# Performance work log

Measured on AMD Instinct MI355X. Metric: run time of the kernel, lower is better.

The kernel has to match this reference:

```python
import math
import jax, jax.numpy as jnp
import numpy as np

FACTOR = 5


def setup_inputs() -> dict:
    key = jax.random.key(0)
    kq, kk, kv, ki = jax.random.split(key, 4)
    B, H, L, D = 4, 8, 2048, 64
    sample_k = min(FACTOR * math.ceil(math.log(L)), L)  # 40
    queries = jax.random.normal(kq, (B, H, L, D), dtype=jnp.float32)
    keys = jax.random.normal(kk, (B, H, L, D), dtype=jnp.float32)
    values = jax.random.normal(kv, (B, H, L, D), dtype=jnp.float32)
    index_sample = jax.random.randint(ki, (L, sample_k), 0, L, dtype=jnp.int64 if jax.config.jax_enable_x64 else jnp.int32)
    return {"queries": queries, "keys": keys, "values": values, "index_sample": index_sample}


def reference(queries, keys, values, index_sample):
    B, H, L_Q, D = queries.shape
    L_K = keys.shape[2]
    u = min(FACTOR * math.ceil(math.log(L_Q)), L_Q)  # n_top queries (= 40)
    scale = 1.0 / math.sqrt(D)

    # --- _prob_QK: sparsity measurement over randomly sampled keys ---
    # K_sample[b,h,q,s,:] = keys[b,h,index_sample[q,s],:]  -> [B,H,L_Q,S,D]
    K_sample = keys[:, :, index_sample, :]
    Q_K_sample = jnp.einsum('bhqd,bhqsd->bhqs', queries, K_sample)  # [B,H,L_Q,S]
    M = Q_K_sample.max(axis=-1) - Q_K_sample.sum(axis=-1) / L_K      # [B,H,L_Q]
    _, M_top = jax.lax.top_k(M, u)                                    # [B,H,u]

    Q_reduce = jnp.take_along_axis(queries, M_top[..., None], axis=2)  # [B,H,u,D]
    scores_top = jnp.einsum('bhud,bhkd->bhuk', Q_reduce, keys) * scale  # [B,H,u,L_K]

    # --- initial context: causal cumulative sum of V (mask_flag=True) ---
    context = jnp.cumsum(values, axis=2)  # [B,H,L_Q,D]

    # --- ProbMask: causal rows gathered at the selected query indices ---
    causal = jnp.triu(jnp.ones((L_Q, L_K), dtype=bool), 1)  # [L_Q,L_K]
    mask = causal[M_top]                                     # [B,H,u,L_K]
    scores_top = jnp.where(mask, -jnp.inf, scores_top)

    attn = jax.nn.softmax(scores_top, axis=-1)                       # [B,H,u,L_K]
    update = jnp.einsum('bhuk,bhkd->bhud', attn, values)             # [B,H,u,D]

    b_idx = jnp.arange(B)[:, None, None]
    h_idx = jnp.arange(H)[None, :, None]
    context = context.at[b_idx, h_idx, M_top].set(update.astype(context.dtype))
    return context
```

## Files before the change

### kernel.cpp

```cpp
#include <hip/hip_runtime.h>
#include <math.h>

#define BB 4
#define HH 8
#define LL 2048
#define DD 64
#define SK 40
#define BH (BB*HH)
#define NG 10

__device__ __forceinline__ unsigned ordu(float v) {
    unsigned u = __float_as_uint(v);
    return (u & 0x80000000u) ? ~u : (u | 0x80000000u);
}

__global__ __launch_bounds__(256) void stage1_kernel(
        const float* __restrict__ Q, const float* __restrict__ K,
        const float* __restrict__ V, const int* __restrict__ IDX,
        float* __restrict__ M, float* __restrict__ csum) {
    int tid = threadIdx.x;
    if (blockIdx.x < 2048) {
        int x = blockIdx.x;
        int bhLo = x & 7;
        int r = x >> 3;
        int bhHi = r & 3;
        int chunk = r >> 2;
        int bh = bhHi * 8 + bhLo;
        int qbase = chunk * 32;
        int w = tid >> 6, lane = tid & 63;
        int c = lane & 3;
        int h = (lane >> 2) & 1;
        int qw = lane >> 3;
        int qi = w * 8 + qw;
        int qpos = qbase + qi;

        __shared__ int sidx[32 * SK];
        for (int i = tid; i < 32 * SK; i += 256) sidx[i] = IDX[(size_t)qbase * SK + i];

        const float4* Q4 = (const float4*)Q;
        const float4* K4 = (const float4*)K;
        float4 qreg[4];
        #pragma unroll
        for (int j = 0; j < 4; ++j)
            qreg[j] = Q4[((size_t)bh * LL + qpos) * 16 + j * 4 + c];
        __syncthreads();

        size_t kb4 = (size_t)bh * LL * 16;
        const int* my = sidx + qi * SK + h * 20;

        int iA = my[0], iB = my[1];
        float4 A[4], B[4];
        #pragma unroll
        for (int j = 0; j < 4; ++j) {
            A[j] = K4[kb4 + (size_t)iA * 16 + j * 4 + c];
            B[j] = K4[kb4 + (size_t)iB * 16 + j * 4 + c];
        }
        int iC = my[2], iD = my[3];

        float mx = -INFINITY, sm = 0.f;
        for (int s = 0; s < 20; s += 2) {
            float4 Cr[4], Dr[4];
            if (s + 2 < 20) {
                #pragma unroll
                for (int j = 0; j < 4; ++j) {
                    Cr[j] = K4[kb4 + (size_t)iC * 16 + j * 4 + c];
                    Dr[j] = K4[kb4 + (size_t)iD * 16 + j * 4 + c];
                }
                if (s + 4 < 20) { iC = my[s + 4]; iD = my[s + 5]; }
            }
            float p0 = 0.f, p1 = 0.f;
            #pragma unroll
            for (int j = 0; j < 4; ++j) {
                p0 += A[j].x * qreg[j].x + A[j].y * qreg[j].y + A[j].z * qreg[j].z + A[j].w * qreg[j].w;
                p1 += B[j].x * qreg[j].x + B[j].y * qreg[j].y + B[j].z * qreg[j].z + B[j].w * qreg[j].w;
            }
            p0 += __shfl_xor(p0, 1, 64);
            p0 += __shfl_xor(p0, 2, 64);
            p1 += __shfl_xor(p1, 1, 64);
            p1 += __shfl_xor(p1, 2, 64);
            mx = fmaxf(mx, fmaxf(p0, p1));
            sm += p0 + p1;
            #pragma unroll
            for (int j = 0; j < 4; ++j) { A[j] = Cr[j]; B[j] = Dr[j]; }
        }
        mx = fmaxf(mx, __shfl_xor(mx, 4, 64));
        sm += __shfl_xor(sm, 4, 64);
        if ((lane & 7) == 0) M[(size_t)bh * LL + qpos] = mx - sm * (1.0f / (float)LL);
    } else {
        int x = blockIdx.x - 2048;
        int bhLo = x & 7, r = x >> 3;
        int bhHi = r & 3, c = r >> 2;
        int bh = bhHi * 8 + bhLo;
        int d = tid & 63, sg = tid >> 6;
        size_t base = (size_t)bh * LL * DD;
        int row0 = c * 128 + sg * 32;
        float s = 0.f;
        for (int j = 0; j < 32; ++j) s += V[base + (size_t)(row0 + j) * DD + d];
        __shared__ float part[4][DD];
        part[sg][d] = s;
        __syncthreads();
        if (sg == 0)
            csum[((size_t)bh * 16 + c) * DD + d] = part[0][d] + part[1][d] + part[2][d] + part[3][d];
    }
}

__global__ __launch_bounds__(256) void stage2_kernel(
        const float* __restrict__ V, const float* __restrict__ csum,
        const float* __restrict__ M, float* __restrict__ out,
        int* __restrict__ topk) {
    int tid = threadIdx.x;
    if (blockIdx.x < 512) {
        int x = blockIdx.x;
        int bhLo = x & 7, r = x >> 3;
        int bhHi = r & 3, c = r >> 2;
        int bh = bhHi * 8 + bhLo;
        int d = tid & 63, sg = tid >> 6;
        size_t base = (size_t)bh * LL * DD;
        int row0 = c * 128 + sg * 32;
        float v[32];
        #pragma unroll
        for (int j = 0; j < 32; ++j) v[j] = V[base + (size_t)(row0 + j) * DD + d];
        float s = 0.f;
        #pragma unroll
        for (int j = 0; j < 32; ++j) s += v[j];
        __shared__ float part[4][DD];
        part[sg][d] = s;
        __syncthreads();
        float pre = 0.f;
        for (int cc = 0; cc < c; ++cc) pre += csum[((size_t)bh * 16 + cc) * DD + d];
        for (int ss = 0; ss < sg; ++ss) pre += part[ss][d];
        float acc = pre;
        #pragma unroll
        for (int j = 0; j < 32; ++j) {
            acc += v[j];
            out[base + (size_t)(row0 + j) * DD + d] = acc;
        }
    } else {
        int bh = blockIdx.x - 512;
        __shared__ unsigned hist[256];
        __shared__ unsigned bc_prefix, bc_need;
        __shared__ unsigned cnt_gt, cnt_eq;
        __shared__ int eqlist[128];
        __shared__ int sel[SK];

        unsigned v[8];
        #pragma unroll
        for (int j = 0; j < 8; ++j)
            v[j] = ordu(M[(size_t)bh * LL + tid + j * 256]);

        unsigned prefix = 0, need = SK;
        #pragma unroll
        for (int pass = 0; pass < 4; ++pass) {
            const int s = 24 - 8 * pass;
            const unsigned maskHigh = (pass == 0) ? 0u : (0xFFFFFFFFu << (s + 8));
            hist[tid] = 0;
            __syncthreads();
            #pragma unroll
            for (int j = 0; j < 8; ++j)
                if (((v[j] ^ prefix) & maskHigh) == 0)
                    atomicAdd(&hist[(v[j] >> s) & 0xFF], 1u);
            __syncthreads();
            unsigned above = 0;
            for (int b = tid + 1; b < 256; ++b) above += hist[b];
            if (above < need && above + hist[tid] >= need) {
                bc_prefix = prefix | ((unsigned)tid << s);
                bc_need = need - above;
            }
            __syncthreads();
            prefix = bc_prefix;
            need = bc_need;
            __syncthreads();
        }
        unsigned T = prefix;
        if (tid == 0) { cnt_gt = 0; cnt_eq = 0; }
        __syncthreads();
        #pragma unroll
        for (int j = 0; j < 8; ++j) {
            int idx = tid + j * 256;
            if (v[j] > T) { unsigned p = atomicAdd(&cnt_gt, 1u); sel[p] = idx; }
            else if (v[j] == T) { unsigned p = atomicAdd(&cnt_eq, 1u); if (p < 128) eqlist[p] = idx; }
        }
        __syncthreads();
        if (tid == 0) {
            int ne = (int)min(cnt_eq, 128u);
            unsigned base = cnt_gt;
            for (unsigned r2 = 0; r2 < need; ++r2) {
                int bj = 0, bv = 0x7FFFFFFF;
                for (int j = 0; j < ne; ++j)
                    if (eqlist[j] < bv) { bv = eqlist[j]; bj = j; }
                sel[base + r2] = bv;
                eqlist[bj] = 0x7FFFFFFF;
            }
        }
        __syncthreads();
        if (tid < SK) {
            int mine = sel[tid];
            int rank = 0;
            #pragma unroll
            for (int j = 0; j < SK; ++j) rank += (sel[j] > mine);
            topk[bh * SK + rank] = mine;
        }
    }
}

__global__ __launch_bounds__(256) void attn_kernel(
        const float* __restrict__ Q, const float* __restrict__ K,
        const float* __restrict__ V, const int* __restrict__ topk,
        float* __restrict__ out) {
    int x = blockIdx.x;
    int bh = x & 31;
    int g = x >> 5;
    int tid = threadIdx.x;

    int qp[4];
    #pragma unroll
    for (int i = 0; i < 4; ++i) qp[i] = topk[bh * SK + g * 4 + i];
    int nk = qp[0] + 1;

    const float4* Q4 = (const float4*)Q;
    const float4* K4 = (const float4*)K;
    const float4* V4 = (const float4*)V;

    int w = tid >> 6, lane = tid & 63;
    int c = lane & 3, kw = lane >> 2;

    float4 qreg[4][4];
    #pragma unroll
    for (int i = 0; i < 4; ++i)
        #pragma unroll
        for (int j = 0; j < 4; ++j)
            qreg[i][j] = Q4[((size_t)bh * LL + qp[i]) * 16 + j * 4 + c];

    __shared__ float sc[4][LL];
    __shared__ float red[4][4], red2[4][4];
    __shared__ float opart[16][16][4];

    size_t kb4 = (size_t)bh * LL * 16;
    int rounds = (nk + 63) >> 6;
    for (int rr = 0; rr < rounds; ++rr) {
        int key = rr * 64 + w * 16 + kw;
        if (key < nk) {
            float4 A[4];
            #pragma unroll
            for (int j = 0; j < 4; ++j) A[j] = K4[kb4 + (size_t)key * 16 + j * 4 + c];
            float p0 = 0.f, p1 = 0.f, p2 = 0.f, p3 = 0.f;
            #pragma unroll
            for (int j = 0; j < 4; ++j) {
                p0 += A[j].x * qreg[0][j].x + A[j].y * qreg[0][j].y + A[j].z * qreg[0][j].z + A[j].w * qreg[0][j].w;
                p1 += A[j].x * qreg[1][j].x + A[j].y * qreg[1][j].y + A[j].z * qreg[1][j].z + A[j].w * qreg[1][j].w;
                p2 += A[j].x * qreg[2][j].x + A[j].y * qreg[2][j].y + A[j].z * qreg[2][j].z + A[j].w * qreg[2][j].w;
                p3 += A[j].x * qreg[3][j].x + A[j].y * qreg[3][j].y + A[j].z * qreg[3][j].z + A[j].w * qreg[3][j].w;
            }
            p0 += __shfl_xor(p0, 1, 64); p0 += __shfl_xor(p0, 2, 64);
            p1 += __shfl_xor(p1, 1, 64); p1 += __shfl_xor(p1, 2, 64);
            p2 += __shfl_xor(p2, 1, 64); p2 += __shfl_xor(p2, 2, 64);
            p3 += __shfl_xor(p3, 1, 64); p3 += __shfl_xor(p3, 2, 64);
            if (c == 0) {
                sc[0][key] = (key <= qp[0]) ? p0 * 0.125f : -INFINITY;
                sc[1][key] = (key <= qp[1]) ? p1 * 0.125f : -INFINITY;
                sc[2][key] = (key <= qp[2]) ? p2 * 0.125f : -INFINITY;
                sc[3][key] = (key <= qp[3]) ? p3 * 0.125f : -INFINITY;
            }
        }
    }
    __syncthreads();

    float m[4] = {-INFINITY, -INFINITY, -INFINITY, -INFINITY};
    for (int j = tid; j < nk; j += 256) {
        #pragma unroll
        for (int i = 0; i < 4; ++i) m[i] = fmaxf(m[i], sc[i][j]);
    }
    #pragma unroll
    for (int i = 0; i < 4; ++i) {
        float mv = m[i];
        #pragma unroll
        for (int off = 32; off > 0; off >>= 1) mv = fmaxf(mv, __shfl_xor(mv, off, 64));
        if (lane == 0) red[w][i] = mv;
        m[i] = mv;
    }
    __syncthreads();
    #pragma unroll
    for (int i = 0; i < 4; ++i)
        m[i] = fmaxf(fmaxf(red[0][i], red[1][i]), fmaxf(red[2][i], red[3][i]));

    float l[4] = {0.f, 0.f, 0.f, 0.f};
    for (int j = tid; j < nk; j += 256) {
        #pragma unroll
        for (int i = 0; i < 4; ++i) {
            float e = expf(sc[i][j] - m[i]);
            sc[i][j] = e;
            l[i] += e;
        }
    }
    #pragma unroll
    for (int i = 0; i < 4; ++i) {
        float lv = l[i];
        #pragma unroll
        for (int off = 32; off > 0; off >>= 1) lv += __shfl_xor(lv, off, 64);
        if (lane == 0) red2[w][i] = lv;
    }
    __syncthreads();
    float linv[4];
    #pragma unroll
    for (int i = 0; i < 4; ++i)
        linv[i] = 1.0f / (red2[0][i] + red2[1][i] + red2[2][i] + red2[3][i]);

    int col4 = tid & 15, kg = tid >> 4;
    float4 acc[4];
    #pragma unroll
    for (int i = 0; i < 4; ++i) acc[i] = make_float4(0.f, 0.f, 0.f, 0.f);
    size_t vb4 = (size_t)bh * LL * 16;
    for (int j = kg; j < nk; j += 16) {
        float4 vv = V4[vb4 + (size_t)j * 16 + col4];
        #pragma unroll
        for (int i = 0; i < 4; ++i) {
            float sj = sc[i][j];
            acc[i].x += sj * vv.x; acc[i].y += sj * vv.y;
            acc[i].z += sj * vv.z; acc[i].w += sj * vv.w;
        }
    }
    #pragma unroll
    for (int i = 0; i < 4; ++i) {
        opart[kg][col4][0] = acc[i].x;
        opart[kg][col4][1] = acc[i].y;
        opart[kg][col4][2] = acc[i].z;
        opart[kg][col4][3] = acc[i].w;
        __syncthreads();
        if (tid < DD) {
            int c4 = tid >> 2, cp = tid & 3;
            float s = 0.f;
            #pragma unroll
            for (int kg2 = 0; kg2 < 16; ++kg2) s += opart[kg2][c4][cp];
            out[((size_t)bh * LL + qp[i]) * DD + tid] = s * linv[i];
        }
        __syncthreads();
    }
}

extern "C" void kernel_launch(void* const* d_in, const int* in_sizes, int n_in,
                              void* d_out, int out_size, void* d_ws, size_t ws_size,
                              hipStream_t stream) {
    const float* Q   = (const float*)d_in[0];
    const float* K   = (const float*)d_in[1];
    const float* V   = (const float*)d_in[2];
    const int*   IDX = (const int*)d_in[3];
    float* out = (float*)d_out;

    char* ws = (char*)d_ws;
    float* M    = (float*)ws;  ws += (size_t)BH * LL * sizeof(float);
    int*   topk = (int*)ws;    ws += ((size_t)BH * SK * sizeof(int) + 255) & ~255ull;
    float* csum = (float*)ws;

    stage1_kernel<<<2560, 256, 0, stream>>>(Q, K, V, IDX, M, csum);
    stage2_kernel<<<544, 256, 0, stream>>>(V, csum, M, out, topk);
    attn_kernel<<<BH * NG, 256, 0, stream>>>(Q, K, V, topk, out);
}
```

Measured before the change: 178.7 us.

## Stream K tiles through shared memory for sampled QK with per-query bucketed indices

The sparsity-measurement part of stage1 now processes 128 queries per block. It streams the whole K for the head through shared memory in 128-row tiles instead of gathering random K rows from global memory. Each query's sample indices are bucketed by tile into shared memory, so each tile only touches the samples that fall in it. This replaces random global gathers with coalesced loads, but every block now reads all of K, many times more bytes, and adds syncs, a serial bucketing pass and divergent per-query loop lengths.

```diff
diff --git a/kernel.cpp b/kernel.cpp
--- a/kernel.cpp
+++ b/kernel.cpp
@@ -8,10 +8,18 @@
 #define SK 40
 #define BH (BB*HH)
 #define NG 10
+#define QB 128
+#define NT 16
+#define TR 128
+#define KPAD 17
 
 __device__ __forceinline__ unsigned ordu(float v) {
     unsigned u = __float_as_uint(v);
     return (u & 0x80000000u) ? ~u : (u | 0x80000000u);
+}
+
+__device__ __forceinline__ float dot4(float4 a, float4 b) {
+    return a.x * b.x + a.y * b.y + a.z * b.z + a.w * b.w;
 }
 
 __global__ __launch_bounds__(256) void stage1_kernel(
@@ -19,75 +27,86 @@
         const float* __restrict__ V, const int* __restrict__ IDX,
         float* __restrict__ M, float* __restrict__ csum) {
     int tid = threadIdx.x;
-    if (blockIdx.x < 2048) {
+    if (blockIdx.x < 512) {
         int x = blockIdx.x;
         int bhLo = x & 7;
         int r = x >> 3;
         int bhHi = r & 3;
-        int chunk = r >> 2;
+        int qc = r >> 2;
         int bh = bhHi * 8 + bhLo;
-        int qbase = chunk * 32;
-        int w = tid >> 6, lane = tid & 63;
-        int c = lane & 3;
-        int h = (lane >> 2) & 1;
-        int qw = lane >> 3;
-        int qi = w * 8 + qw;
-        int qpos = qbase + qi;
-
-        __shared__ int sidx[32 * SK];
-        for (int i = tid; i < 32 * SK; i += 256) sidx[i] = IDX[(size_t)qbase * SK + i];
-
+        int qbase = qc * QB;
+
+        __shared__ float4 ktile[TR * KPAD];
+        __shared__ unsigned short sorted[QB][SK];
+        __shared__ unsigned short starts[QB][NT + 1];
+
+        int* raw = (int*)ktile;
+        for (int i = tid; i < QB * SK; i += 256) raw[i] = IDX[(size_t)qbase * SK + i];
+        __syncthreads();
+
+        if (tid < QB) {
+            int pos = 0;
+            const int* myraw = raw + tid * SK;
+            for (int t = 0; t < NT; ++t) {
+                starts[tid][t] = (unsigned short)pos;
+                for (int s = 0; s < SK; ++s) {
+                    int ks = myraw[s];
+                    if ((ks >> 7) == t) sorted[tid][pos++] = (unsigned short)ks;
+                }
+            }
+            starts[tid][NT] = (unsigned short)pos;
+        }
+
+        int g = tid >> 2, c = tid & 3;
+        int q0 = qbase + g, q1 = qbase + g + 64;
         const float4* Q4 = (const float4*)Q;
         const float4* K4 = (const float4*)K;
-        float4 qreg[4];
-        #pragma unroll
-        for (int j = 0; j < 4; ++j)
-            qreg[j] = Q4[((size_t)bh * LL + qpos) * 16 + j * 4 + c];
-        __syncthreads();
+        float4 qa[4], qb[4];
+        #pragma unroll
+        for (int j = 0; j < 4; ++j) {
+            qa[j] = Q4[((size_t)bh * LL + q0) * 16 + j * 4 + c];
+            qb[j] = Q4[((size_t)bh * LL + q1) * 16 + j * 4 + c];
+        }
 
         size_t kb4 = (size_t)bh * LL * 16;
-        const int* my = sidx + qi * SK + h * 20;
-
-        int iA = my[0], iB = my[1];
-        float4 A[4], B[4];
-        #pragma unroll
-        for (int j = 0; j < 4; ++j) {
-            A[j] = K4[kb4 + (size_t)iA * 16 + j * 4 + c];
-            B[j] = K4[kb4 + (size_t)iB * 16 + j * 4 + c];
-        }
-        int iC = my[2], iD = my[3];
-
-        float mx = -INFINITY, sm = 0.f;
-        for (int s = 0; s < 20; s += 2) {
-            float4 Cr[4], Dr[4];
-            if (s + 2 < 20) {
-                #pragma unroll
-                for (int j = 0; j < 4; ++j) {
-                    Cr[j] = K4[kb4 + (size_t)iC * 16 + j * 4 + c];
-                    Dr[j] = K4[kb4 + (size_t)iD * 16 + j * 4 + c];
-                }
-                if (s + 4 < 20) { iC = my[s + 4]; iD = my[s + 5]; }
-            }
-            float p0 = 0.f, p1 = 0.f;
-            #pragma unroll
-            for (int j = 0; j < 4; ++j) {
-                p0 += A[j].x * qreg[j].x + A[j].y * qreg[j].y + A[j].z * qreg[j].z + A[j].w * qreg[j].w;
-                p1 += B[j].x * qreg[j].x + B[j].y * qreg[j].y + B[j].z * qreg[j].z + B[j].w * qreg[j].w;
-            }
-            p0 += __shfl_xor(p0, 1, 64);
-            p0 += __shfl_xor(p0, 2, 64);
-            p1 += __shfl_xor(p1, 1, 64);
-            p1 += __shfl_xor(p1, 2, 64);
-            mx = fmaxf(mx, fmaxf(p0, p1));
-            sm += p0 + p1;
-            #pragma unroll
-            for (int j = 0; j < 4; ++j) { A[j] = Cr[j]; B[j] = Dr[j]; }
-        }
-        mx = fmaxf(mx, __shfl_xor(mx, 4, 64));
-        sm += __shfl_xor(sm, 4, 64);
-        if ((lane & 7) == 0) M[(size_t)bh * LL + qpos] = mx - sm * (1.0f / (float)LL);
+        float mxa = -INFINITY, sma = 0.f, mxb = -INFINITY, smb = 0.f;
+
+        for (int kt = 0; kt < NT; ++kt) {
+            __syncthreads();
+            #pragma unroll
+            for (int i = 0; i < 8; ++i) {
+                int f = tid + i * 256;
+                int row = f >> 4, ch = f & 15;
+                ktile[row * KPAD + ch] = K4[kb4 + (size_t)(kt * TR + row) * 16 + ch];
+            }
+            __syncthreads();
+            int s0 = starts[g][kt], s1 = starts[g][kt + 1];
+            for (int s = s0; s < s1; ++s) {
+                int rowi = sorted[g][s] & (TR - 1);
+                const float4* kr = ktile + rowi * KPAD;
+                float p = dot4(kr[c], qa[0]) + dot4(kr[4 + c], qa[1])
+                        + dot4(kr[8 + c], qa[2]) + dot4(kr[12 + c], qa[3]);
+                p += __shfl_xor(p, 1, 64);
+                p += __shfl_xor(p, 2, 64);
+                mxa = fmaxf(mxa, p); sma += p;
+            }
+            int t0 = starts[g + 64][kt], t1 = starts[g + 64][kt + 1];
+            for (int s = t0; s < t1; ++s) {
+                int rowi = sorted[g + 64][s] & (TR - 1);
+                const float4* kr = ktile + rowi * KPAD;
+                float p = dot4(kr[c], qb[0]) + dot4(kr[4 + c], qb[1])
+                        + dot4(kr[8 + c], qb[2]) + dot4(kr[12 + c], qb[3]);
+                p += __shfl_xor(p, 1, 64);
+                p += __shfl_xor(p, 2, 64);
+                mxb = fmaxf(mxb, p); smb += p;
+            }
+        }
+        if (c == 0) {
+            M[(size_t)bh * LL + q0] = mxa - sma * (1.0f / (float)LL);
+            M[(size_t)bh * LL + q1] = mxb - smb * (1.0f / (float)LL);
+        }
     } else {
-        int x = blockIdx.x - 2048;
+        int x = blockIdx.x - 512;
         int bhLo = x & 7, r = x >> 3;
         int bhHi = r & 3, c = r >> 2;
         int bh = bhHi * 8 + bhLo;
@@ -246,10 +265,10 @@
             float p0 = 0.f, p1 = 0.f, p2 = 0.f, p3 = 0.f;
             #pragma unroll
             for (int j = 0; j < 4; ++j) {
-                p0 += A[j].x * qreg[0][j].x + A[j].y * qreg[0][j].y + A[j].z * qreg[0][j].z + A[j].w * qreg[0][j].w;
-                p1 += A[j].x * qreg[1][j].x + A[j].y * qreg[1][j].y + A[j].z * qreg[1][j].z + A[j].w * qreg[1][j].w;
-                p2 += A[j].x * qreg[2][j].x + A[j].y * qreg[2][j].y + A[j].z * qreg[2][j].z + A[j].w * qreg[2][j].w;
-                p3 += A[j].x * qreg[3][j].x + A[j].y * qreg[3][j].y + A[j].z * qreg[3][j].z + A[j].w * qreg[3][j].w;
+                p0 += dot4(A[j], qreg[0][j]);
+                p1 += dot4(A[j], qreg[1][j]);
+                p2 += dot4(A[j], qreg[2][j]);
+                p3 += dot4(A[j], qreg[3][j]);
             }
             p0 += __shfl_xor(p0, 1, 64); p0 += __shfl_xor(p0, 2, 64);
             p1 += __shfl_xor(p1, 1, 64); p1 += __shfl_xor(p1, 2, 64);
@@ -276,7 +295,6 @@
         #pragma unroll
         for (int off = 32; off > 0; off >>= 1) mv = fmaxf(mv, __shfl_xor(mv, off, 64));
         if (lane == 0) red[w][i] = mv;
-        m[i] = mv;
     }
     __syncthreads();
     #pragma unroll
@@ -351,7 +369,7 @@
     int*   topk = (int*)ws;    ws += ((size_t)BH * SK * sizeof(int) + 255) & ~255ull;
     float* csum = (float*)ws;
 
-    stage1_kernel<<<2560, 256, 0, stream>>>(Q, K, V, IDX, M, csum);
+    stage1_kernel<<<1024, 256, 0, stream>>>(Q, K, V, IDX, M, csum);
     stage2_kernel<<<544, 256, 0, stream>>>(V, csum, M, out, topk);
     attn_kernel<<<BH * NG, 256, 0, stream>>>(Q, K, V, topk, out);
 }
```

Result: slower. 221.5 us (+24.0%).
